# Optimization experiments

Measured on AMD Instinct MI355X. Metric: run time of the kernel, lower is better.

The kernel has to match this reference:

```python
import jax, jax.numpy as jnp
import numpy as np

B, N, E = 64, 2048, 32768          # graphs, nodes/graph, edges/graph
DIM = 64
RATIO = 0.8
K1 = int(np.ceil(RATIO * N))        # 1639 nodes/graph after pool1
K2 = int(np.ceil(RATIO * K1))       # 1312 nodes/graph after pool2
NUM_CLASSES = 6


def gcn_conv(x, W, b, src, dst, valid, n):
    # GCNConv with self-loops: out = D^-1/2 (A+I) D^-1/2 (x W) + b
    xw = x @ W                                          # [n, DIM]
    deg = jnp.zeros(n, x.dtype).at[dst].add(valid) + 1.0  # in-degree incl. self-loop
    norm = valid * jax.lax.rsqrt(deg[src] * deg[dst])      # per-edge norm (0 for masked)
    agg = jnp.zeros_like(xw).at[dst].add(xw[src] * norm[:, None])
    return agg + xw / deg[:, None] + b                  # self-loop term has norm 1/deg


def topk_pool(x, p, n_graphs, n_per, k):
    # PyG TopKPooling: score = tanh(x.p/||p||); keep top-k per graph; gate x by score
    score = jnp.tanh((x @ p) / jnp.linalg.norm(p))       # [n_graphs*n_per]
    vals, idx = jax.lax.top_k(score.reshape(n_graphs, n_per), k)  # [n_graphs, k]
    xg = x.reshape(n_graphs, n_per, -1)
    sel = jnp.take_along_axis(xg, idx[..., None], axis=1)          # [n_graphs, k, DIM]
    xp = sel * vals[..., None]
    perm = (idx + (jnp.arange(n_graphs) * n_per)[:, None]).reshape(-1)  # global ids kept
    return xp.reshape(n_graphs * k, -1), perm


def global_max_mean(x, n_graphs, n_per):
    xg = x.reshape(n_graphs, n_per, -1)
    return jnp.concatenate([xg.max(axis=1), xg.mean(axis=1)], axis=1)  # [n_graphs, 2*DIM]


def forward(x, edge_index, batch, W1, b1, p1, W2, b2, p2, lin1_w, lin1_b, lin2_w, lin2_b):
    src, dst = edge_index[0], edge_index[1]
    n_total = B * N
    ones = jnp.ones(src.shape[0], x.dtype)

    x = jax.nn.relu(gcn_conv(x, W1, b1, src, dst, ones, n_total))
    x, perm = topk_pool(x, p1, B, N, K1)
    x1 = global_max_mean(x, B, K1)

    # filter_adj: reindex edges to surviving nodes; drop (mask) edges touching removed nodes
    new_id = jnp.full(n_total, -1, jnp.int32).at[perm].set(jnp.arange(B * K1, dtype=jnp.int32))
    s2, d2 = new_id[src], new_id[dst]
    valid = ((s2 >= 0) & (d2 >= 0)).astype(x.dtype)
    s2 = jnp.where(s2 >= 0, s2, 0)
    d2 = jnp.where(d2 >= 0, d2, 0)

    x = jax.nn.relu(gcn_conv(x, W2, b2, s2, d2, valid, B * K1))
    x, _ = topk_pool(x, p2, B, K1, K2)
    x2 = global_max_mean(x, B, K2)

    h = x1 + x2
    h = jax.nn.relu(h @ lin1_w + lin1_b)
    return h @ lin2_w + lin2_b                           # [B, NUM_CLASSES]


def setup_inputs():
    key = jax.random.key(0)
    ks = jax.random.split(key, 10)
    x = jax.random.normal(ks[0], (B * N, DIM), jnp.float32)
    off = (jnp.arange(B) * N)[:, None]
    src = (jax.random.randint(ks[1], (B, E), 0, N) + off).reshape(-1)
    dst = (jax.random.randint(ks[2], (B, E), 0, N) + off).reshape(-1)
    edge_index = jnp.stack([src, dst]).astype(jnp.int32)
    batch = jnp.repeat(jnp.arange(B, dtype=jnp.int32), N)
    s = 1.0 / np.sqrt(DIM)
    return {
        "x": x,
        "edge_index": edge_index,
        "batch": batch,
        "W1": jax.random.normal(ks[3], (DIM, DIM), jnp.float32) * s,
        "b1": jnp.zeros(DIM, jnp.float32),
        "p1": jax.random.normal(ks[4], (DIM,), jnp.float32) * s,
        "W2": jax.random.normal(ks[5], (DIM, DIM), jnp.float32) * s,
        "b2": jnp.zeros(DIM, jnp.float32),
        "p2": jax.random.normal(ks[6], (DIM,), jnp.float32) * s,
        "lin1_w": jax.random.normal(ks[7], (2 * DIM, DIM), jnp.float32) / np.sqrt(2 * DIM),
        "lin1_b": jnp.zeros(DIM, jnp.float32),
        "lin2_w": jax.random.normal(ks[8], (DIM, NUM_CLASSES), jnp.float32) * s,
        "lin2_b": jnp.zeros(NUM_CLASSES, jnp.float32),
    }


def reference(x, edge_index, batch, W1, b1, p1, W2, b2, p2, lin1_w, lin1_b, lin2_w, lin2_b):
    return forward(x, edge_index, batch, W1, b1, p1, W2, b2, p2, lin1_w, lin1_b, lin2_w, lin2_b)
```

## Files before the change

### kernel.cpp

```cpp
#include <hip/hip_runtime.h>
#include <hip/hip_bf16.h>
#include <cstdint>
#include <cstddef>

#define B_    64
#define N_    2048
#define E_    32768
#define DIM_  64
#define K1_   1639
#define K2_   1312
#define NTOT  (B_ * N_)
#define ETOT  (B_ * E_)
#define N2TOT (B_ * K1_)
#define NCLS  6
#define PB_   8
#define CHUNKS_ 16
#define SLICES_ 16
#define BCAP  3072
#define REG_  192

typedef float f4 __attribute__((ext_vector_type(4)));
typedef _Float16 h2 __attribute__((ext_vector_type(2)));
typedef _Float16 h8 __attribute__((ext_vector_type(8)));

static __device__ __forceinline__ float fdot2(h2 a, h2 b, float c) {
    return __builtin_amdgcn_fdot2(a, b, c, false);
}
static __device__ __forceinline__ h2 pkrtz(float a, float b) {
    return __builtin_bit_cast(h2, __builtin_amdgcn_cvt_pkrtz(a, b));
}
static __device__ __forceinline__ unsigned long long mk_key(float s, int i) {
    unsigned u = __float_as_uint(s);
    u = (u & 0x80000000u) ? ~u : (u | 0x80000000u);
    return ((unsigned long long)u << 11) | (unsigned long long)(2047 - i);
}

__launch_bounds__(128)
__global__ void k_wprep(const float* W1, const float* W2, h8* wf) {
    int t = threadIdx.x;
    int stage = t >> 6, lane = t & 63;
    const float* W = stage ? W2 : W1;
    int q = lane >> 4, c = lane & 15;
#pragma unroll
    for (int ks = 0; ks < 2; ks++)
#pragma unroll
        for (int nt = 0; nt < 4; nt++) {
            h8 h, l;
#pragma unroll
            for (int j = 0; j < 8; j++) {
                float wv = W[(ks * 32 + q * 8 + j) * 64 + nt * 16 + c];
                _Float16 hh = (_Float16)wv;
                h[j] = hh;
                l[j] = (_Float16)(wv - (float)hh);
            }
            wf[(size_t)stage * 1024 + (((ks * 4 + nt) * 2 + 0) * 64) + lane] = h;
            wf[(size_t)stage * 1024 + (((ks * 4 + nt) * 2 + 1) * 64) + lane] = l;
        }
}

template<int STAGE>
__launch_bounds__(256)
__global__ void k_bucket(const int* src, const int* dst, const int* remap,
                         int* bcnt, unsigned int* blist) {
    const int LSTR = (STAGE == 1) ? 128 : 103;
    __shared__ unsigned int lb[CHUNKS_][REG_];
    __shared__ int lc[CHUNKS_];
    __shared__ int rm[N_];
    int b = blockIdx.x;
    int g = b & 63, slice = b >> 6;
    int tid = threadIdx.x;
    if (tid < CHUNKS_) lc[tid] = 0;
    if (STAGE == 2)
        for (int i = tid; i < N_; i += 256) rm[i] = remap[g * N_ + i];
    __syncthreads();
    const int ESL = E_ / SLICES_;
    const int* sp = src + (size_t)g * E_ + slice * ESL;
    const int* dp = dst + (size_t)g * E_ + slice * ESL;
    int gbase = g * ((STAGE == 1) ? N_ : K1_);
    for (int e = tid * 4; e < ESL; e += 1024) {
        int4 ss = *(const int4*)&sp[e];
        int4 dd = *(const int4*)&dp[e];
#pragma unroll
        for (int t = 0; t < 4; t++) {
            int s = (&ss.x)[t], d = (&dd.x)[t];
            if (STAGE == 2) {
                s = rm[s & (N_ - 1)]; d = rm[d & (N_ - 1)];
                if ((s | d) < 0) continue;
                s -= gbase; d -= gbase;
            } else {
                s &= (N_ - 1); d &= (N_ - 1);
            }
            int ch = d / LSTR;
            int dl = d - ch * LSTR;
            int p = atomicAdd(&lc[ch], 1);
            if (p < REG_) lb[ch][p] = ((unsigned)dl << 12) | (unsigned)s;
        }
    }
    __syncthreads();
    for (int ch = 0; ch < CHUNKS_; ch++) {
        int n = min(lc[ch], REG_);
        unsigned int* out = blist + (size_t)(g * CHUNKS_ + ch) * BCAP + slice * REG_;
        for (int i = tid; i < n; i += 256) out[i] = lb[ch][i];
    }
    if (tid < CHUNKS_) bcnt[(g * SLICES_ + slice) * CHUNKS_ + tid] = min(lc[tid], REG_);
}

template<int STAGE>
__launch_bounds__(256)
__global__ void k_sort(const int* bcnt, unsigned int* blist,
                       const float* xf, const unsigned int* xg,
                       unsigned int* xb, int* ninfo) {
    const int NL   = (STAGE == 1) ? N_ : K1_;
    const int LSTR = (STAGE == 1) ? 128 : 103;
    __shared__ int cnt[128], st[128], cur[128], cnt_s[SLICES_], stot[2];
    __shared__ float rsqv[128];
    __shared__ unsigned short sorted[BCAP];
    int b = blockIdx.x;
    int g = b & 63, ch = b >> 6;
    int tid = threadIdx.x;
    if (tid < 128) { cnt[tid] = 0; cur[tid] = 0; }
    if (tid < SLICES_) cnt_s[tid] = bcnt[(g * SLICES_ + tid) * CHUNKS_ + ch];
    __syncthreads();
    size_t bb = (size_t)(g * CHUNKS_ + ch) * BCAP;
    const unsigned int* bl = blist + bb;
    const int TOT = SLICES_ * REG_;
    for (int i = tid; i < TOT; i += 256) {
        int s = i / REG_, j = i - s * REG_;
        if (j < cnt_s[s]) atomicAdd(&cnt[bl[i] >> 12], 1);
    }
    __syncthreads();
    if (tid < 128) {
        int v = cnt[tid];
        int l64 = tid & 63;
#pragma unroll
        for (int o = 1; o < 64; o <<= 1) {
            int t = __shfl_up(v, o);
            if (l64 >= o) v += t;
        }
        st[tid] = v;
        if (l64 == 63) stot[tid >> 6] = v;
    }
    __syncthreads();
    if (tid >= 64 && tid < 128) st[tid] += stot[0];
    __syncthreads();
    for (int i = tid; i < TOT; i += 256) {
        int s = i / REG_, j = i - s * REG_;
        if (j < cnt_s[s]) {
            unsigned pk = bl[i];
            int dl = (int)(pk >> 12);
            int p = st[dl] - cnt[dl] + atomicAdd(&cur[dl], 1);
            sorted[p] = (unsigned short)(pk & 0xFFFu);
        }
    }
    __syncthreads();
    int n = st[127];
    for (int i = tid; i < n; i += 256) blist[bb + i] = ((unsigned int)sorted[i]) << 7;
    int lo = ch * LSTR;
    int nloc = min(LSTR, NL - lo);
    int gbase = g * NL;
    if (tid < nloc) {
        int node = gbase + lo + tid;
        int c = cnt[tid];
        int start = (int)bb + st[tid] - c;
        ninfo[node] = (start << 8) | min(c, 255);
        rsqv[tid] = rsqrtf((float)(c + 1));
    }
    __syncthreads();
    for (int idx = tid; idx < nloc * 32; idx += 256) {
        int nl = idx >> 5, f2 = idx & 31;
        int node = gbase + lo + nl;
        float sc = rsqv[nl];
        float2 v;
        if (STAGE == 1) {
            v = ((const float2*)xf)[(size_t)node * 32 + f2];
        } else {
            h2 hv = __builtin_bit_cast(h2, xg[(size_t)node * 32 + f2]);
            v.x = (float)hv.x; v.y = (float)hv.y;
        }
        h2 o = {(_Float16)(v.x * sc), (_Float16)(v.y * sc)};
        xb[(size_t)node * 32 + f2] = __builtin_bit_cast(unsigned int, o);
    }
}

template<bool GATE>
__launch_bounds__(256, 4)
__global__ void k_aggconv(const unsigned int* xb, const int* ninfo, const unsigned int* csr,
                          const h8* wfrag, const float* bias, const float* pvec,
                          float* y, float* score) {
    __shared__ float4 ls4[1024];
    __shared__ h8 wlds[2][4][2][64];
    float* ls = (float*)ls4;
    int b = blockIdx.x;
    int wg;
    if (GATE) {
        int xcd = b & 7, k = b >> 3;
        wg = (xcd < 7 ? xcd * 205 : 1435 + (xcd - 7) * 204) + k;
    } else {
        wg = (b & 7) * 256 + (b >> 3);
    }
    int tid = threadIdx.x;
    int wid = tid >> 6, lane = tid & 63;
    int half = lane >> 5, l32 = lane & 31, hbase = half << 5;
    int l32_4 = l32 << 2;
    int rowbase = wg * 64 + wid * 16;

    {
        const h8* wsrc = wfrag + (GATE ? 1024 : 0);
        h8* wd = (h8*)wlds;
        for (int i = tid; i < 1024; i += 256) wd[i] = wsrc[i];
    }

    const char* xbb = (const char*)xb;
    const h2 one0  = {(_Float16)1.0f, (_Float16)0.0f};
    const h2 zero1 = {(_Float16)0.0f, (_Float16)1.0f};
    int g0 = 0, bnd = 0;
    if (GATE) { g0 = (wg * 64) / K1_; bnd = (g0 + 1) * K1_; }
    auto gbyte = [&](int node) -> int {
        if (GATE) { int gr = (node >= bnd) ? (g0 + 1) : g0; return gr * (K1_ * 128); }
        return (node & ~(N_ - 1)) << 7;
    };

    int niv = 0;
    if (lane < 16) niv = ninfo[rowbase + lane];
    int ni = __shfl(niv, half);
    int gbb = gbyte(rowbase + half);
    int sv = 0;
    { int c0 = ni & 255; if (l32 < c0) sv = (int)csr[(ni >> 8) + l32] + gbb; }
#pragma unroll 1
    for (int p = 0; p < 8; p++) {
        int cnt = ni & 255, base = ni >> 8;
        int ni_n = 0, sv_n = 0, gbb_n = 0;
        if (p < 7) {
            ni_n = __shfl(niv, 2 * (p + 1) + half);
            gbb_n = gbyte(rowbase + 2 * (p + 1) + half);
            int cn = ni_n & 255;
            if (l32 < cn) sv_n = (int)csr[(ni_n >> 8) + l32] + gbb_n;
        }
        int rloc = wid * 16 + 2 * p + half;
        int node = wg * 64 + rloc;
        unsigned selfu = *(const unsigned*)(xbb + (unsigned)(node * 128 + l32_4));
        float acx[4] = {0.f, 0.f, 0.f, 0.f};
        float acy[4] = {0.f, 0.f, 0.f, 0.f};
        int svc = sv;
        for (int chunk = 0; chunk < cnt; chunk += 32) {
            int nch = min(32, cnt - chunk);
            if (chunk) svc = (l32 < nch) ? (int)csr[base + chunk + l32] + gbb : 0;
            int i = 0;
            for (; i + 16 <= nch; i += 16) {
                int e[16]; unsigned u[16];
#pragma unroll
                for (int k = 0; k < 16; k++) e[k] = __shfl(svc, hbase + i + k);
#pragma unroll
                for (int k = 0; k < 16; k++)
                    u[k] = *(const unsigned*)(xbb + (unsigned)(e[k] + l32_4));
#pragma unroll
                for (int k = 0; k < 16; k++) {
                    h2 h = __builtin_bit_cast(h2, u[k]);
                    acx[k & 3] = fdot2(h, one0,  acx[k & 3]);
                    acy[k & 3] = fdot2(h, zero1, acy[k & 3]);
                }
            }
            for (; i + 8 <= nch; i += 8) {
                int e[8]; unsigned u[8];
#pragma unroll
                for (int k = 0; k < 8; k++) e[k] = __shfl(svc, hbase + i + k);
#pragma unroll
                for (int k = 0; k < 8; k++)
                    u[k] = *(const unsigned*)(xbb + (unsigned)(e[k] + l32_4));
#pragma unroll
                for (int k = 0; k < 8; k++) {
                    h2 h = __builtin_bit_cast(h2, u[k]);
                    acx[k & 3] = fdot2(h, one0,  acx[k & 3]);
                    acy[k & 3] = fdot2(h, zero1, acy[k & 3]);
                }
            }
            for (; i + 4 <= nch; i += 4) {
                int e[4]; unsigned u[4];
#pragma unroll
                for (int k = 0; k < 4; k++) e[k] = __shfl(svc, hbase + i + k);
#pragma unroll
                for (int k = 0; k < 4; k++)
                    u[k] = *(const unsigned*)(xbb + (unsigned)(e[k] + l32_4));
#pragma unroll
                for (int k = 0; k < 4; k++) {
                    h2 h = __builtin_bit_cast(h2, u[k]);
                    acx[k] = fdot2(h, one0,  acx[k]);
                    acy[k] = fdot2(h, zero1, acy[k]);
                }
            }
            for (; i < nch; i++) {
                int e = __shfl(svc, hbase + i);
                h2 h = __builtin_bit_cast(h2, *(const unsigned*)(xbb + (unsigned)(e + l32_4)));
                acx[0] = fdot2(h, one0,  acx[0]);
                acy[0] = fdot2(h, zero1, acy[0]);
            }
        }
        {
            h2 sh = __builtin_bit_cast(h2, selfu);
            acx[0] = fdot2(sh, one0,  acx[0]);
            acy[0] = fdot2(sh, zero1, acy[0]);
        }
        float rd = rsqrtf((float)(cnt + 1));
        float2 o;
        o.x = ((acx[0] + acx[1]) + (acx[2] + acx[3])) * rd;
        o.y = ((acy[0] + acy[1]) + (acy[2] + acy[3])) * rd;
        int pi = rloc * 32 + ((((l32 >> 1) ^ (rloc & 7)) << 1) | (l32 & 1));
        ((float2*)ls)[pi] = o;
        ni = ni_n; sv = sv_n; gbb = gbb_n;
    }
    __syncthreads();

    int q = lane >> 4, c = lane & 15;
    int rl16 = (wid * 16 + c) * 16;
    int cx = c & 7;
    h8 ah[2], al[2];
#pragma unroll
    for (int ks = 0; ks < 2; ks++) {
        float4 v0 = ls4[rl16 + ((ks * 8 + q * 2 + 0) ^ cx)];
        float4 v1 = ls4[rl16 + ((ks * 8 + q * 2 + 1) ^ cx)];
        float vv[8] = {v0.x, v0.y, v0.z, v0.w, v1.x, v1.y, v1.z, v1.w};
        h8 h, l;
#pragma unroll
        for (int j = 0; j < 8; j += 2) {
            h2 hp = pkrtz(vv[j], vv[j + 1]);
            float r0 = vv[j]     - (float)hp.x;
            float r1 = vv[j + 1] - (float)hp.y;
            h2 lp = pkrtz(r0, r1);
            h[j] = hp.x; h[j + 1] = hp.y;
            l[j] = lp.x; l[j + 1] = lp.y;
        }
        ah[ks] = h; al[ks] = l;
    }
    float pp = 0.f;
#pragma unroll
    for (int i = 0; i < DIM_; i++) pp += pvec[i] * pvec[i];
    float rpn = rsqrtf(pp);
    float dot[4] = {0.f, 0.f, 0.f, 0.f};
#pragma unroll
    for (int nt = 0; nt < 4; nt++) {
        f4 acc = {0.f, 0.f, 0.f, 0.f};
#pragma unroll
        for (int ks = 0; ks < 2; ks++) {
            h8 wh = wlds[ks][nt][0][lane];
            h8 wl = wlds[ks][nt][1][lane];
            acc = __builtin_amdgcn_mfma_f32_16x16x32_f16(ah[ks], wh, acc, 0, 0, 0);
            acc = __builtin_amdgcn_mfma_f32_16x16x32_f16(ah[ks], wl, acc, 0, 0, 0);
            acc = __builtin_amdgcn_mfma_f32_16x16x32_f16(al[ks], wh, acc, 0, 0, 0);
        }
        float bcol = bias[nt * 16 + c];
        float pcol = pvec[nt * 16 + c];
        float st[4];
#pragma unroll
        for (int reg = 0; reg < 4; reg++) {
            float v = fmaxf(acc[reg] + bcol, 0.f);
            st[reg] = v;
            dot[reg] += v * pcol;
        }
#pragma unroll
        for (int reg = 0; reg < 4; reg++)
            y[(size_t)(wg * 64 + wid * 16 + q * 4 + reg) * DIM_ + nt * 16 + c] = st[reg];
    }
#pragma unroll
    for (int m = 1; m < 16; m <<= 1) {
#pragma unroll
        for (int reg = 0; reg < 4; reg++) dot[reg] += __shfl_xor(dot[reg], m);
    }
    if (c == 0) {
#pragma unroll
        for (int reg = 0; reg < 4; reg++)
            score[wg * 64 + wid * 16 + q * 4 + reg] = tanhf(dot[reg] * rpn);
    }
}

template<int STAGE>
__launch_bounds__(256)
__global__ void k_thresh(const float* score, unsigned long long* thresh) {
    const int Nin = (STAGE == 1) ? N_ : K1_;
    const int K   = (STAGE == 1) ? K1_ : K2_;
    __shared__ unsigned long long keys[N_];
    __shared__ int bins[256], wsum[4];
    __shared__ unsigned long long s_prefix;
    __shared__ int s_need;
    int g = blockIdx.x, tid = threadIdx.x;
    int l64 = tid & 63, wid = tid >> 6;
    const float* sg = score + (size_t)g * Nin;
    for (int i = tid; i < Nin; i += 256) keys[i] = mk_key(sg[i], i);
    if (tid == 0) { s_need = K; s_prefix = 0ull; }
    __syncthreads();
    for (int shift = 40; shift >= 0; shift -= 8) {
        bins[tid] = 0;
        __syncthreads();
        unsigned long long pref = s_prefix;
        int need = s_need;
        int hi = shift + 8;
        for (int i = tid; i < Nin; i += 256) {
            unsigned long long k = keys[i];
            if ((k >> hi) == pref) atomicAdd(&bins[(int)((k >> shift) & 255)], 1);
        }
        __syncthreads();
        int mine = bins[tid];
        int v = mine;
#pragma unroll
        for (int o = 1; o < 64; o <<= 1) {
            int t = __shfl_down(v, o);
            if (l64 + o < 64) v += t;
        }
        if (l64 == 0) wsum[wid] = v;
        __syncthreads();
        for (int w = wid + 1; w < 4; w++) v += wsum[w];
        int nxt = v - mine;
        if (v >= need && nxt < need) {
            s_prefix = (pref << 8) | (unsigned long long)tid;
            s_need = need - nxt;
        }
        __syncthreads();
    }
    if (tid == 0) thresh[g] = s_prefix;
}

template<int STAGE>
__launch_bounds__(256)
__global__ void k_pool(const float* score, const float* conv, const unsigned long long* thresh,
                       int* new_id, unsigned int* xg, float* part) {
    const int Nin = (STAGE == 1) ? N_ : K1_;
    const int RNG = (STAGE == 1) ? (N_ / PB_) : ((K1_ + PB_ - 1) / PB_);
    __shared__ int rnk[256];
    __shared__ unsigned char keepf[256];
    __shared__ int wsum[4], s_base[4];
    __shared__ float rmx[4][64], rsm[4][64];
    int b = blockIdx.x;
    int g = b & 63, pb = b >> 6;
    int tid = threadIdx.x;
    int l64 = tid & 63, wid = tid >> 6;
    const float* sg = score + (size_t)g * Nin;
    unsigned long long T = thresh[g];
    int R0 = pb * RNG;
    int R1 = min(R0 + RNG, Nin);
    if (STAGE == 1) {
        int cb = 0;
        for (int i = tid; i < R0; i += 256) cb += (mk_key(sg[i], i) >= T) ? 1 : 0;
#pragma unroll
        for (int o = 32; o; o >>= 1) cb += __shfl_down(cb, o);
        if (l64 == 0) s_base[wid] = cb;
        int i = R0 + tid;
        int keep = (i < R1 && mk_key(sg[i], i) >= T) ? 1 : 0;
        keepf[tid] = (unsigned char)keep;
        int v = keep;
#pragma unroll
        for (int o = 1; o < 64; o <<= 1) {
            int t = __shfl_up(v, o);
            if (l64 >= o) v += t;
        }
        if (l64 == 63) wsum[wid] = v;
        __syncthreads();
        int base = s_base[0] + s_base[1] + s_base[2] + s_base[3];
        int wbase = 0;
        for (int w = 0; w < wid; w++) wbase += wsum[w];
        int r = base + wbase + v - keep;
        rnk[tid] = r;
        if (i < Nin) new_id[g * N_ + i] = keep ? (g * K1_ + r) : -1;
    } else {
        int i = R0 + tid;
        keepf[tid] = (unsigned char)((i < R1 && mk_key(sg[i], i) >= T) ? 1 : 0);
    }
    __syncthreads();
    float mx = -3.402823466e38f, sm = 0.f;
    for (int i = R0 + wid; i < R1; i += 4) {
        if (!keepf[i - R0]) continue;
        float val = sg[i];
        float v = conv[(size_t)(g * Nin + i) * DIM_ + l64] * val;
        mx = fmaxf(mx, v);
        sm += v;
        if (STAGE == 1) {
            float vo = __shfl_xor(v, 1);
            if (!(l64 & 1)) {
                h2 pk2 = {(_Float16)v, (_Float16)vo};
                xg[(size_t)(g * K1_ + rnk[i - R0]) * 32 + (l64 >> 1)] =
                    __builtin_bit_cast(unsigned int, pk2);
            }
        }
    }
    rmx[wid][l64] = mx; rsm[wid][l64] = sm;
    __syncthreads();
    if (wid == 0) {
        mx = fmaxf(fmaxf(rmx[0][l64], rmx[1][l64]), fmaxf(rmx[2][l64], rmx[3][l64]));
        sm = rsm[0][l64] + rsm[1][l64] + rsm[2][l64] + rsm[3][l64];
        part[((size_t)(g * PB_ + pb) * 2 + 0) * 64 + l64] = mx;
        part[((size_t)(g * PB_ + pb) * 2 + 1) * 64 + l64] = sm;
    }
}

__launch_bounds__(64)
__global__ void k_head(const float* part1, const float* part2,
                       const float* l1w, const float* l1b,
                       const float* l2w, const float* l2b, float* out) {
    __shared__ float h[128];
    __shared__ float h1[64];
    int g = blockIdx.x, t = threadIdx.x;
    float mx1 = -3.402823466e38f, sm1 = 0.f, mx2 = -3.402823466e38f, sm2 = 0.f;
#pragma unroll
    for (int c = 0; c < PB_; c++) {
        mx1 = fmaxf(mx1, part1[((size_t)(g * PB_ + c) * 2 + 0) * 64 + t]);
        sm1 += part1[((size_t)(g * PB_ + c) * 2 + 1) * 64 + t];
        mx2 = fmaxf(mx2, part2[((size_t)(g * PB_ + c) * 2 + 0) * 64 + t]);
        sm2 += part2[((size_t)(g * PB_ + c) * 2 + 1) * 64 + t];
    }
    h[t]      = mx1 + mx2;
    h[t + 64] = sm1 / (float)K1_ + sm2 / (float)K2_;
    __syncthreads();
    float acc = l1b[t];
#pragma unroll 8
    for (int i = 0; i < 128; i++) acc += h[i] * l1w[i * 64 + t];
    h1[t] = fmaxf(acc, 0.0f);
    __syncthreads();
    if (t < NCLS) {
        float o = l2b[t];
#pragma unroll
        for (int i = 0; i < 64; i++) o += h1[i] * l2w[i * NCLS + t];
        out[g * NCLS + t] = o;
    }
}

extern "C" void kernel_launch(void* const* d_in, const int* in_sizes, int n_in,
                              void* d_out, int out_size, void* d_ws, size_t ws_size,
                              hipStream_t stream) {
    const float* x   = (const float*)d_in[0];
    const int*   ei  = (const int*)d_in[1];
    const int*   src = ei;
    const int*   dst = ei + ETOT;
    const float* W1  = (const float*)d_in[3];
    const float* b1  = (const float*)d_in[4];
    const float* p1  = (const float*)d_in[5];
    const float* W2  = (const float*)d_in[6];
    const float* b2  = (const float*)d_in[7];
    const float* p2  = (const float*)d_in[8];
    const float* l1w = (const float*)d_in[9];
    const float* l1b = (const float*)d_in[10];
    const float* l2w = (const float*)d_in[11];
    const float* l2b = (const float*)d_in[12];
    (void)in_sizes; (void)n_in; (void)out_size; (void)ws_size;

    char* ws = (char*)d_ws;
    size_t off = 0;
    auto alloc = [&](size_t bytes) -> void* {
        void* p = ws + off;
        off = (off + bytes + 255) & ~(size_t)255;
        return p;
    };
    float*              bufA   = (float*)             alloc((size_t)NTOT  * DIM_ * 4);
    float*              bufB   = (float*)             alloc((size_t)N2TOT * DIM_ * 4);
    unsigned int*       blist  = (unsigned int*)      alloc((size_t)B_ * CHUNKS_ * BCAP * 4);
    unsigned int*       xb     = (unsigned int*)      alloc((size_t)NTOT * 32 * 4);
    int*                bcnt   = (int*)               alloc((size_t)B_ * SLICES_ * CHUNKS_ * 4);
    int*                ninfo  = (int*)               alloc((size_t)NTOT * 4);
    float*              score  = (float*)             alloc((size_t)NTOT * 4);
    int*                newid  = (int*)               alloc((size_t)NTOT * 4);
    unsigned long long* thr    = (unsigned long long*)alloc((size_t)B_ * 8);
    float*              part1  = (float*)             alloc((size_t)B_ * PB_ * 128 * 4);
    float*              part2  = (float*)             alloc((size_t)B_ * PB_ * 128 * 4);
    h8*                 wfrag  = (h8*)                alloc((size_t)2048 * 16);
    unsigned int*       xg     = (unsigned int*)bufB;

    k_wprep<<<1, 128, 0, stream>>>(W1, W2, wfrag);

    k_bucket<1><<<B_ * SLICES_, 256, 0, stream>>>(src, dst, nullptr, bcnt, blist);
    k_sort<1><<<B_ * CHUNKS_, 256, 0, stream>>>(bcnt, blist, x, nullptr, xb, ninfo);
    k_aggconv<false><<<NTOT / 64, 256, 0, stream>>>(xb, ninfo, blist, wfrag, b1, p1, bufA, score);
    k_thresh<1><<<B_, 256, 0, stream>>>(score, thr);
    k_pool<1><<<B_ * PB_, 256, 0, stream>>>(score, bufA, thr, newid, xg, part1);

    k_bucket<2><<<B_ * SLICES_, 256, 0, stream>>>(src, dst, newid, bcnt, blist);
    k_sort<2><<<B_ * CHUNKS_, 256, 0, stream>>>(bcnt, blist, nullptr, xg, xb, ninfo);
    k_aggconv<true><<<N2TOT / 64, 256, 0, stream>>>(xb, ninfo, blist, wfrag, b2, p2, bufB, score);
    k_thresh<2><<<B_, 256, 0, stream>>>(score, thr);
    k_pool<2><<<B_ * PB_, 256, 0, stream>>>(score, bufB, thr, nullptr, nullptr, part2);

    k_head<<<B_, 64, 0, stream>>>(part1, part2, l1w, l1b, l2w, l2b, (float*)d_out);
}
```

Measured before the change: 316.6 us.

## Gather neighbor rows with wave-uniform scalar CSR indices, one node per wave

The aggregation loop now processes one node per wave iteration (16 iterations) instead of two nodes per iteration split across half-waves. Neighbor indices are read through readfirstlane as wave-uniform scalar loads rather than being loaded per lane and broadcast with shuffles. The cross-iteration prefetch of the next node's CSR entries is dropped, and the accumulators are reduced from four to two. Both 32-lane halves compute the same row and only the lower half writes it, so half the lanes do redundant gather work in exchange for less shuffle and VGPR overhead.

```diff
diff --git a/kernel.cpp b/kernel.cpp
--- a/kernel.cpp
+++ b/kernel.cpp
@@ -200,9 +200,7 @@
     }
     int tid = threadIdx.x;
     int wid = tid >> 6, lane = tid & 63;
-    int half = lane >> 5, l32 = lane & 31, hbase = half << 5;
-    int l32_4 = l32 << 2;
-    int rowbase = wg * 64 + wid * 16;
+    int half = lane >> 5, l32 = lane & 31;
 
     {
         const h8* wsrc = wfrag + (GATE ? 1024 : 0);
@@ -213,100 +211,61 @@
     const char* xbb = (const char*)xb;
     const h2 one0  = {(_Float16)1.0f, (_Float16)0.0f};
     const h2 zero1 = {(_Float16)0.0f, (_Float16)1.0f};
+    int rb = __builtin_amdgcn_readfirstlane(wg * 64 + wid * 16);
     int g0 = 0, bnd = 0;
     if (GATE) { g0 = (wg * 64) / K1_; bnd = (g0 + 1) * K1_; }
-    auto gbyte = [&](int node) -> int {
-        if (GATE) { int gr = (node >= bnd) ? (g0 + 1) : g0; return gr * (K1_ * 128); }
-        return (node & ~(N_ - 1)) << 7;
-    };
-
-    int niv = 0;
-    if (lane < 16) niv = ninfo[rowbase + lane];
-    int ni = __shfl(niv, half);
-    int gbb = gbyte(rowbase + half);
-    int sv = 0;
-    { int c0 = ni & 255; if (l32 < c0) sv = (int)csr[(ni >> 8) + l32] + gbb; }
+
 #pragma unroll 1
-    for (int p = 0; p < 8; p++) {
-        int cnt = ni & 255, base = ni >> 8;
-        int ni_n = 0, sv_n = 0, gbb_n = 0;
-        if (p < 7) {
-            ni_n = __shfl(niv, 2 * (p + 1) + half);
-            gbb_n = gbyte(rowbase + 2 * (p + 1) + half);
-            int cn = ni_n & 255;
-            if (l32 < cn) sv_n = (int)csr[(ni_n >> 8) + l32] + gbb_n;
-        }
-        int rloc = wid * 16 + 2 * p + half;
-        int node = wg * 64 + rloc;
-        unsigned selfu = *(const unsigned*)(xbb + (unsigned)(node * 128 + l32_4));
-        float acx[4] = {0.f, 0.f, 0.f, 0.f};
-        float acy[4] = {0.f, 0.f, 0.f, 0.f};
-        int svc = sv;
-        for (int chunk = 0; chunk < cnt; chunk += 32) {
-            int nch = min(32, cnt - chunk);
-            if (chunk) svc = (l32 < nch) ? (int)csr[base + chunk + l32] + gbb : 0;
-            int i = 0;
-            for (; i + 16 <= nch; i += 16) {
-                int e[16]; unsigned u[16];
-#pragma unroll
-                for (int k = 0; k < 16; k++) e[k] = __shfl(svc, hbase + i + k);
-#pragma unroll
-                for (int k = 0; k < 16; k++)
-                    u[k] = *(const unsigned*)(xbb + (unsigned)(e[k] + l32_4));
-#pragma unroll
-                for (int k = 0; k < 16; k++) {
-                    h2 h = __builtin_bit_cast(h2, u[k]);
-                    acx[k & 3] = fdot2(h, one0,  acx[k & 3]);
-                    acy[k & 3] = fdot2(h, zero1, acy[k & 3]);
-                }
+    for (int p = 0; p < 16; p++) {
+        int node = rb + p;
+        int ni = __builtin_amdgcn_readfirstlane(ninfo[node]);
+        int cnt = ni & 255;
+        int base = ni >> 8;
+        int gbb;
+        if (GATE) { int gr = (node >= bnd) ? (g0 + 1) : g0; gbb = gr * (K1_ * 128); }
+        else       gbb = (node & ~(N_ - 1)) << 7;
+        const unsigned* csrg = csr + base;
+        const char* gx = xbb + gbb;
+        const unsigned* srp = (const unsigned*)(xbb + (size_t)(unsigned)node * 128);
+        unsigned selfu = srp[l32];
+        float ax0 = 0.f, ax1 = 0.f, ay0 = 0.f, ay1 = 0.f;
+        int j = 0;
+        for (; j + 8 <= cnt; j += 8) {
+            unsigned ro[8];
+#pragma unroll
+            for (int k = 0; k < 8; k++)
+                ro[k] = __builtin_amdgcn_readfirstlane(csrg[j + k]);
+            unsigned u[8];
+#pragma unroll
+            for (int k = 0; k < 8; k++)
+                u[k] = ((const unsigned*)(gx + ro[k]))[l32];
+#pragma unroll
+            for (int k = 0; k < 8; k++) {
+                h2 h = __builtin_bit_cast(h2, u[k]);
+                if (k & 1) { ax1 = fdot2(h, one0, ax1); ay1 = fdot2(h, zero1, ay1); }
+                else       { ax0 = fdot2(h, one0, ax0); ay0 = fdot2(h, zero1, ay0); }
             }
-            for (; i + 8 <= nch; i += 8) {
-                int e[8]; unsigned u[8];
-#pragma unroll
-                for (int k = 0; k < 8; k++) e[k] = __shfl(svc, hbase + i + k);
-#pragma unroll
-                for (int k = 0; k < 8; k++)
-                    u[k] = *(const unsigned*)(xbb + (unsigned)(e[k] + l32_4));
-#pragma unroll
-                for (int k = 0; k < 8; k++) {
-                    h2 h = __builtin_bit_cast(h2, u[k]);
-                    acx[k & 3] = fdot2(h, one0,  acx[k & 3]);
-                    acy[k & 3] = fdot2(h, zero1, acy[k & 3]);
-                }
-            }
-            for (; i + 4 <= nch; i += 4) {
-                int e[4]; unsigned u[4];
-#pragma unroll
-                for (int k = 0; k < 4; k++) e[k] = __shfl(svc, hbase + i + k);
-#pragma unroll
-                for (int k = 0; k < 4; k++)
-                    u[k] = *(const unsigned*)(xbb + (unsigned)(e[k] + l32_4));
-#pragma unroll
-                for (int k = 0; k < 4; k++) {
-                    h2 h = __builtin_bit_cast(h2, u[k]);
-                    acx[k] = fdot2(h, one0,  acx[k]);
-                    acy[k] = fdot2(h, zero1, acy[k]);
-                }
-            }
-            for (; i < nch; i++) {
-                int e = __shfl(svc, hbase + i);
-                h2 h = __builtin_bit_cast(h2, *(const unsigned*)(xbb + (unsigned)(e + l32_4)));
-                acx[0] = fdot2(h, one0,  acx[0]);
-                acy[0] = fdot2(h, zero1, acy[0]);
-            }
+        }
+        for (; j < cnt; j++) {
+            unsigned ro = __builtin_amdgcn_readfirstlane(csrg[j]);
+            h2 h = __builtin_bit_cast(h2, ((const unsigned*)(gx + ro))[l32]);
+            ax0 = fdot2(h, one0, ax0);
+            ay0 = fdot2(h, zero1, ay0);
         }
         {
             h2 sh = __builtin_bit_cast(h2, selfu);
-            acx[0] = fdot2(sh, one0,  acx[0]);
-            acy[0] = fdot2(sh, zero1, acy[0]);
+            ax0 = fdot2(sh, one0, ax0);
+            ay0 = fdot2(sh, zero1, ay0);
         }
         float rd = rsqrtf((float)(cnt + 1));
         float2 o;
-        o.x = ((acx[0] + acx[1]) + (acx[2] + acx[3])) * rd;
-        o.y = ((acy[0] + acy[1]) + (acy[2] + acy[3])) * rd;
-        int pi = rloc * 32 + ((((l32 >> 1) ^ (rloc & 7)) << 1) | (l32 & 1));
-        ((float2*)ls)[pi] = o;
-        ni = ni_n; sv = sv_n; gbb = gbb_n;
+        o.x = (ax0 + ax1) * rd;
+        o.y = (ay0 + ay1) * rd;
+        if (half == 0) {
+            int rloc = wid * 16 + p;
+            int pi = rloc * 32 + ((((l32 >> 1) ^ (rloc & 7)) << 1) | (l32 & 1));
+            ((float2*)ls)[pi] = o;
+        }
     }
     __syncthreads();
 
```

Result: slower. 351.0 us (+10.9%).
